# Performance work log

Measured on AMD Instinct MI355X. Metric: run time of the kernel, lower is better.

## Reference

```python
import jax, jax.numpy as jnp
import numpy as np
import math

DEGREE = 4   # MacLaurin expansion degree
FEAT = 8     # input feature dim F
BATCH = 65536


def _build_terms_facs():
    """Enumerate all exponent multi-indices with total degree <= DEGREE,
    mirroring the TF meshgrid construction, plus 1/k! factors per term."""
    d1 = DEGREE + 1
    grids = np.meshgrid(*([np.arange(d1)] * FEAT), indexing='ij')
    terms = np.stack(grids, axis=-1).reshape(-1, FEAT)           # [(d+1)^F, F]
    terms = terms[terms.sum(axis=-1) <= DEGREE]                  # [T, F], T = C(F+d, d)
    fact = np.array([math.factorial(k) for k in range(d1)], dtype=np.float32)
    facs = (1.0 / fact)[terms.sum(axis=-1)]                      # [T] = 1/|alpha|!
    return jnp.asarray(terms, dtype=jnp.float32), jnp.asarray(facs, dtype=jnp.float32)


def setup_inputs() -> dict:
    key = jax.random.key(0)
    k1, k2 = jax.random.split(key)
    terms, facs = _build_terms_facs()
    T = terms.shape[0]  # 495
    x = jax.random.uniform(k1, (BATCH, FEAT), dtype=jnp.float32)  # positive inputs (pow-safe)
    coefs = jax.random.normal(k2, (1, T), dtype=jnp.float32) * 0.05
    return {"x": x, "terms": terms, "coefs": coefs, "facs": facs}


def reference(x, terms, coefs, facs):
    # monomials: prod_f x[b,f]^terms[t,f]  -> [B, T]
    mono = jnp.prod(x[:, None, :] ** terms[None, :, :], axis=-1)
    # weighted sum over terms: sum_t facs[t] * coefs[0,t] * mono[b,t] -> [B]
    return jnp.sum(facs * coefs * mono, axis=-1)
```

## Files before the change

kernel.cpp:

```cpp
#include <hip/hip_runtime.h>

#define NF 8
#define DEG 4
#define NTERMS 495

constexpr long long nCkll(int n, int k) {
    long long r = 1;
    for (int i = 1; i <= k; ++i) r = r * (n - k + i) / i;
    return r;
}
constexpr int subcnt(int F, int REM) { return (int)nCkll(NF - F + REM, REM); }

template<int F, int REM, int T0> struct Node;
template<int F, int REM, int E, int T0> struct Branch;

template<int F, int REM, int T0>
struct Node {
    static __device__ __forceinline__ void run(const float* xs, const float4* w4,
                                               float4& wq, float p, float* acc) {
        Branch<F, REM, 0, T0>::run(xs, w4, wq, p, acc);
    }
};

template<int REM, int T0>
struct Node<NF, REM, T0> {
    static __device__ __forceinline__ void run(const float*, const float4* w4,
                                               float4& wq, float p, float* acc) {
        if constexpr ((T0 & 3) == 0) {
            wq = w4[T0 / 4];
        }
        constexpr int c = T0 & 3;
        float wv = (c == 0) ? wq.x : (c == 1) ? wq.y : (c == 2) ? wq.z : wq.w;
        acc[c] = fmaf(wv, p, acc[c]);
    }
};

template<int F, int REM, int E, int T0>
struct Branch {
    static constexpr int childCnt = subcnt(F + 1, REM - E);
    static __device__ __forceinline__ void run(const float* xs, const float4* w4,
                                               float4& wq, float pf, float* acc) {
        Node<F + 1, REM - E, T0>::run(xs, w4, wq, pf, acc);
        if constexpr (E < REM) {
            Branch<F, REM, E + 1, T0 + childCnt>::run(xs, w4, wq, pf * xs[F], acc);
        }
    }
};

__global__ __launch_bounds__(256)
void maclaurin_fused(const float* __restrict__ x,
                     const float* __restrict__ coefs,
                     const float* __restrict__ facs,
                     float* __restrict__ out, int n) {
    __shared__ __align__(16) float wl[496];

    const int tid = threadIdx.x;
    const int b   = blockIdx.x * blockDim.x + tid;

    float xs[NF];
    if (b < n) {
        const float4* xp = (const float4*)(x + (size_t)b * NF);
        float4 v0 = xp[0];
        float4 v1 = xp[1];
        xs[0] = v0.x; xs[1] = v0.y; xs[2] = v0.z; xs[3] = v0.w;
        xs[4] = v1.x; xs[5] = v1.y; xs[6] = v1.z; xs[7] = v1.w;
    }

    if (tid < 123) {
        float4 c = ((const float4*)coefs)[tid];
        float4 f = ((const float4*)facs)[tid];
        ((float4*)wl)[tid] = make_float4(c.x * f.x, c.y * f.y, c.z * f.z, c.w * f.w);
    } else if (tid < 126) {
        int i = 492 + (tid - 123);
        wl[i] = coefs[i] * facs[i];
    } else if (tid == 126) {
        wl[495] = 0.0f;
    }
    __syncthreads();

    if (b >= n) return;

    float acc[4] = {0.0f, 0.0f, 0.0f, 0.0f};
    float4 wq;
    Node<0, DEG, 0>::run(xs, (const float4*)wl, wq, 1.0f, acc);

    out[b] = (acc[0] + acc[1]) + (acc[2] + acc[3]);
}

extern "C" void kernel_launch(void* const* d_in, const int* in_sizes, int n_in,
                              void* d_out, int out_size, void* d_ws, size_t ws_size,
                              hipStream_t stream) {
    const float* x     = (const float*)d_in[0];
    const float* coefs = (const float*)d_in[2];
    const float* facs  = (const float*)d_in[3];
    float* out = (float*)d_out;

    int n = in_sizes[0] / NF;

    maclaurin_fused<<<(n + 255) / 256, 256, 0, stream>>>(x, coefs, facs, out, n);
}
```

Baseline: 9.661 us.

## Evaluate multivariate polynomial with nested Horner scheme instead of monomial expansion

Replaces the explicit enumeration of monomials (a running product times a weight, accumulated into four partial sums) with a recursive Horner evaluation per variable, traversing terms in reverse order. The shared-memory weight vector loads are re-triggered at the top of each float4 group because of the reverse traversal. This cuts the per-term multiply count and the live product registers, at the cost of one long serial FMA dependency chain instead of four independent accumulators.

Result: faster. 9.401 us (-2.7%).

```diff
diff --git a/kernel.cpp b/kernel.cpp
--- a/kernel.cpp
+++ b/kernel.cpp
@@ -11,39 +11,47 @@
 }
 constexpr int subcnt(int F, int REM) { return (int)nCkll(NF - F + REM, REM); }
 
-template<int F, int REM, int T0> struct Node;
-template<int F, int REM, int E, int T0> struct Branch;
+constexpr int csum(int F, int REM, int E) {
+    int s = 0;
+    for (int j = 0; j < E; ++j) s += subcnt(F + 1, REM - j);
+    return s;
+}
+
+template<int F, int REM, int T0> struct HNode;
+template<int F, int REM, int E, int T0> struct HChain;
 
 template<int F, int REM, int T0>
-struct Node {
-    static __device__ __forceinline__ void run(const float* xs, const float4* w4,
-                                               float4& wq, float p, float* acc) {
-        Branch<F, REM, 0, T0>::run(xs, w4, wq, p, acc);
+struct HNode {
+    static __device__ __forceinline__ float eval(const float* xs, const float4* w4,
+                                                 float4& wq) {
+        float acc = HNode<F + 1, 0, T0 + csum(F, REM, REM)>::eval(xs, w4, wq);
+        if constexpr (REM > 0)
+            acc = HChain<F, REM, REM - 1, T0>::step(acc, xs, w4, wq);
+        return acc;
     }
 };
 
 template<int REM, int T0>
-struct Node<NF, REM, T0> {
-    static __device__ __forceinline__ void run(const float*, const float4* w4,
-                                               float4& wq, float p, float* acc) {
-        if constexpr ((T0 & 3) == 0) {
-            wq = w4[T0 / 4];
-        }
+struct HNode<NF, REM, T0> {
+    static __device__ __forceinline__ float eval(const float*, const float4* w4,
+                                                 float4& wq) {
+        if constexpr ((T0 & 3) == 3 || T0 == NTERMS - 1)
+            wq = w4[T0 >> 2];
         constexpr int c = T0 & 3;
-        float wv = (c == 0) ? wq.x : (c == 1) ? wq.y : (c == 2) ? wq.z : wq.w;
-        acc[c] = fmaf(wv, p, acc[c]);
+        return (c == 0) ? wq.x : (c == 1) ? wq.y : (c == 2) ? wq.z : wq.w;
     }
 };
 
 template<int F, int REM, int E, int T0>
-struct Branch {
-    static constexpr int childCnt = subcnt(F + 1, REM - E);
-    static __device__ __forceinline__ void run(const float* xs, const float4* w4,
-                                               float4& wq, float pf, float* acc) {
-        Node<F + 1, REM - E, T0>::run(xs, w4, wq, pf, acc);
-        if constexpr (E < REM) {
-            Branch<F, REM, E + 1, T0 + childCnt>::run(xs, w4, wq, pf * xs[F], acc);
-        }
+struct HChain {
+    static __device__ __forceinline__ float step(float acc, const float* xs,
+                                                 const float4* w4, float4& wq) {
+        float c = HNode<F + 1, REM - E, T0 + csum(F, REM, E)>::eval(xs, w4, wq);
+        acc = fmaf(acc, xs[F], c);
+        if constexpr (E > 0)
+            return HChain<F, REM, E - 1, T0>::step(acc, xs, w4, wq);
+        else
+            return acc;
     }
 };
 
@@ -80,11 +88,10 @@
 
     if (b >= n) return;
 
-    float acc[4] = {0.0f, 0.0f, 0.0f, 0.0f};
     float4 wq;
-    Node<0, DEG, 0>::run(xs, (const float4*)wl, wq, 1.0f, acc);
+    float r = HNode<0, DEG, 0>::eval(xs, (const float4*)wl, wq);
 
-    out[b] = (acc[0] + acc[1]) + (acc[2] + acc[3]);
+    out[b] = r;
 }
 
 extern "C" void kernel_launch(void* const* d_in, const int* in_sizes, int n_in,
```
